# Performance work log

Measured on AMD Instinct MI355X. Metric: run time of the kernel, lower is better.

The kernel has to match this reference:

```python
import jax, jax.numpy as jnp
import numpy as np

B, S, IN_F, OUT_F = 4, 2048, 4096, 4096
ALPHA = 0.01

def setup_inputs() -> dict:
    key = jax.random.key(0)
    k1, k2 = jax.random.split(key, 2)
    # int8-valued activations and weights (stored as int32 per harness dtype)
    x = jax.random.randint(k1, (B, S, IN_F), -127, 127, dtype=jnp.int32)
    weight = jax.random.randint(k2, (IN_F, OUT_F), -127, 127, dtype=jnp.int32)
    bias = jnp.zeros((1, OUT_F), dtype=jnp.float16)
    alpha = jnp.full((1,), ALPHA, dtype=jnp.float32)
    return {"x": x, "weight": weight, "bias": bias, "alpha": alpha}

def reference(x, weight, bias, alpha):
    # Faithful to forward's default (non-hybrid) path:
    # y = F.linear(x.float(), weight.t().float(), bias.float()) * alpha
    # F.linear(x, W^T) == x @ W, with W shape (in_features, out_features).
    x_shape = x.shape
    xf = x.reshape(-1, x_shape[-1]).astype(jnp.float32)          # [B*S, in]
    wf = weight.astype(jnp.float32)                               # [in, out]
    y = (xf @ wf + bias.astype(jnp.float32)) * alpha              # [B*S, out]
    return y.reshape(*x_shape[:-1], -1)                           # [B, S, out]
```

## Files before the change

### kernel.cpp

```cpp
#include <hip/hip_runtime.h>
#include <hip/hip_fp16.h>

using i32x4  = __attribute__((ext_vector_type(4)))  int;
using i32x16 = __attribute__((ext_vector_type(16))) int;

static constexpr int M  = 4 * 2048;
static constexpr int N  = 4096;
static constexpr int K  = 4096;
static constexpr int BM = 128, BN = 128, BK = 64;
static constexpr int NT = K / BK;
static constexpr int TILE = BM * BK;


__device__ __forceinline__ unsigned pack4(i32x4 v) {
  return (unsigned)((v.x & 255) | ((v.y & 255) << 8) | ((v.z & 255) << 16) | (v.w << 24));
}

__global__ __launch_bounds__(256) void pack_x_kernel(const int* __restrict__ x,
                                                     unsigned char* __restrict__ wa) {
  unsigned g = blockIdx.x * 256 + threadIdx.x;
  unsigned tile = g >> 9, gt = g & 511;
  unsigned kg = gt >> 7, row = gt & 127;
  unsigned br = tile >> 6, kt = tile & 63;
  const int* src = x + ((size_t)(br * 128 + row) * K + kt * 64 + kg * 16);
  i32x4 v0 = *(const i32x4*)(src + 0);
  i32x4 v1 = *(const i32x4*)(src + 4);
  i32x4 v2 = *(const i32x4*)(src + 8);
  i32x4 v3 = *(const i32x4*)(src + 12);
  i32x4 d;
  d.x = (int)pack4(v0); d.y = (int)pack4(v1); d.z = (int)pack4(v2); d.w = (int)pack4(v3);
  *(i32x4*)(wa + (size_t)g * 16) = d;
}

__global__ __launch_bounds__(256) void pack_w_kernel(const int* __restrict__ w,
                                                     unsigned char* __restrict__ wb) {
  unsigned g = blockIdx.x * 256 + threadIdx.x;
  unsigned tile = g >> 9, gt = g & 511;
  unsigned kg = gt >> 7, col = gt & 127;
  unsigned bn = tile >> 6, kt = tile & 63;
  unsigned n  = bn * 128 + col;
  unsigned k0 = kt * 64 + kg * 16;
  const int* src = w + (size_t)k0 * N + n;
  i32x4 d;
#pragma unroll
  for (int j = 0; j < 4; ++j) {
    int b0 = src[(size_t)(j * 4 + 0) * N];
    int b1 = src[(size_t)(j * 4 + 1) * N];
    int b2 = src[(size_t)(j * 4 + 2) * N];
    int b3 = src[(size_t)(j * 4 + 3) * N];
    d[j] = (b0 & 255) | ((b1 & 255) << 8) | ((b2 & 255) << 16) | (b3 << 24);
  }
  *(i32x4*)(wb + (size_t)g * 16) = d;
}


__global__ __launch_bounds__(256) void gemm_i8(const unsigned char* __restrict__ wa,
                                               const unsigned char* __restrict__ wb,
                                               const __half* __restrict__ bias,
                                               const float* __restrict__ alphaP,
                                               float* __restrict__ out) {
  __shared__ __align__(16) unsigned char As[2][TILE];
  __shared__ __align__(16) unsigned char Bs[2][TILE];

  const int tid  = threadIdx.x;
  const int lane = tid & 63;
  const int w    = tid >> 6;
  const int wr   = w >> 1, wc = w & 1;
  const int l31  = lane & 31;
  const int kgl  = lane >> 5;

  const int bc = blockIdx.x;
  const int br = blockIdx.y;

  const unsigned char* ga = wa + (size_t)br * NT * TILE;
  const unsigned char* gb = wb + (size_t)bc * NT * TILE;

  i32x4 s0, s1, s2, s3;

#define GLOAD(T) do {                                                \
    const i32x4* ap = (const i32x4*)(ga + (size_t)(T) * TILE);       \
    const i32x4* bp = (const i32x4*)(gb + (size_t)(T) * TILE);       \
    s0 = ap[tid]; s1 = ap[tid + 256];                                \
    s2 = bp[tid]; s3 = bp[tid + 256];                                \
  } while (0)

#define SWRITE(BUF) do {                                             \
    i32x4* aw = (i32x4*)&As[BUF][0];                                 \
    i32x4* bw = (i32x4*)&Bs[BUF][0];                                 \
    aw[tid] = s0; aw[tid + 256] = s1;                                \
    bw[tid] = s2; bw[tid + 256] = s3;                                \
  } while (0)

  GLOAD(0);
  SWRITE(0);
  __syncthreads();

  i32x16 acc[2][2] = {};

  const int arow = wr * 64 + l31;
  const int bcol = wc * 64 + l31;

  for (int t = 0; t < NT; ++t) {
    const int cur = t & 1;
    if (t + 1 < NT) GLOAD(t + 1);

    const unsigned char* Ab = &As[cur][0] + kgl * 2048;
    const unsigned char* Bb = &Bs[cur][0] + kgl * 2048;
#pragma unroll
    for (int kc = 0; kc < 2; ++kc) {
      const unsigned char* Ap = Ab + kc * 4096;
      const unsigned char* Bp = Bb + kc * 4096;
      i32x4 a0 = *(const i32x4*)(Ap + (arow +  0) * 16);
      i32x4 a1 = *(const i32x4*)(Ap + (arow + 32) * 16);
      i32x4 b0 = *(const i32x4*)(Bp + (bcol +  0) * 16);
      i32x4 b1 = *(const i32x4*)(Bp + (bcol + 32) * 16);
      acc[0][0] = __builtin_amdgcn_mfma_i32_32x32x32_i8(a0, b0, acc[0][0], 0, 0, 0);
      acc[0][1] = __builtin_amdgcn_mfma_i32_32x32x32_i8(a0, b1, acc[0][1], 0, 0, 0);
      acc[1][0] = __builtin_amdgcn_mfma_i32_32x32x32_i8(a1, b0, acc[1][0], 0, 0, 0);
      acc[1][1] = __builtin_amdgcn_mfma_i32_32x32x32_i8(a1, b1, acc[1][1], 0, 0, 0);
    }

    __builtin_amdgcn_sched_barrier(0);
    if (t + 1 < NT) SWRITE(cur ^ 1);
    __syncthreads();
  }

  const float alpha = *alphaP;
  const int row0 = br * 128 + wr * 64 + 4 * kgl;
  const int col0 = bc * 128 + wc * 64 + l31;
#pragma unroll
  for (int ni = 0; ni < 2; ++ni) {
    const int col = col0 + ni * 32;
    const float bf = __half2float(bias[col]);
#pragma unroll
    for (int mi = 0; mi < 2; ++mi) {
#pragma unroll
      for (int r = 0; r < 16; ++r) {
        const int row = row0 + mi * 32 + (r & 3) + 8 * (r >> 2);
        out[(size_t)row * N + col] = ((float)acc[mi][ni][r] + bf) * alpha;
      }
    }
  }
#undef GLOAD
#undef SWRITE
}

extern "C" void kernel_launch(void* const* d_in, const int* in_sizes, int n_in,
                              void* d_out, int out_size, void* d_ws, size_t ws_size,
                              hipStream_t stream) {
  const int*    x     = (const int*)d_in[0];
  const int*    wgt   = (const int*)d_in[1];
  const __half* bias  = (const __half*)d_in[2];
  const float*  alpha = (const float*)d_in[3];
  float*        out   = (float*)d_out;

  unsigned char* wa = (unsigned char*)d_ws;
  unsigned char* wb = wa + (size_t)M * K;

  pack_x_kernel<<<(M * (size_t)K / 16) / 256, 256, 0, stream>>>(x, wa);
  pack_w_kernel<<<(N * (size_t)K / 16) / 256, 256, 0, stream>>>(wgt, wb);

  dim3 grid(N / BN, M / BM);
  gemm_i8<<<grid, 256, 0, stream>>>(wa, wb, bias, alpha, out);
}
```

Baseline: 230.4 us.

## Load B fragments directly to registers and merge pack kernels into one launch

The GEMM no longer stages the B tile through shared memory. Each wave loads its B MFMA fragments directly from the pre-packed global buffer into double-buffered registers, prefetched one k-tile ahead, with the main loop unrolled by two to select the register parity. This cuts LDS writes and reads and halves shared-memory usage, but duplicates B reads from global/L2 across waves and adds register pressure. The two packing kernels are also fused into one launch to remove a kernel boundary.

```diff
diff --git a/kernel.cpp b/kernel.cpp
--- a/kernel.cpp
+++ b/kernel.cpp
@@ -11,46 +11,49 @@
 static constexpr int NT = K / BK;
 static constexpr int TILE = BM * BK;
 
+static constexpr int PX_BLOCKS = (int)((size_t)M * K / 16 / 256);
+static constexpr int PW_BLOCKS = (int)((size_t)N * K / 16 / 256);
 
 __device__ __forceinline__ unsigned pack4(i32x4 v) {
   return (unsigned)((v.x & 255) | ((v.y & 255) << 8) | ((v.z & 255) << 16) | (v.w << 24));
 }
 
-__global__ __launch_bounds__(256) void pack_x_kernel(const int* __restrict__ x,
-                                                     unsigned char* __restrict__ wa) {
-  unsigned g = blockIdx.x * 256 + threadIdx.x;
-  unsigned tile = g >> 9, gt = g & 511;
-  unsigned kg = gt >> 7, row = gt & 127;
-  unsigned br = tile >> 6, kt = tile & 63;
-  const int* src = x + ((size_t)(br * 128 + row) * K + kt * 64 + kg * 16);
-  i32x4 v0 = *(const i32x4*)(src + 0);
-  i32x4 v1 = *(const i32x4*)(src + 4);
-  i32x4 v2 = *(const i32x4*)(src + 8);
-  i32x4 v3 = *(const i32x4*)(src + 12);
-  i32x4 d;
-  d.x = (int)pack4(v0); d.y = (int)pack4(v1); d.z = (int)pack4(v2); d.w = (int)pack4(v3);
-  *(i32x4*)(wa + (size_t)g * 16) = d;
-}
-
-__global__ __launch_bounds__(256) void pack_w_kernel(const int* __restrict__ w,
-                                                     unsigned char* __restrict__ wb) {
-  unsigned g = blockIdx.x * 256 + threadIdx.x;
-  unsigned tile = g >> 9, gt = g & 511;
-  unsigned kg = gt >> 7, col = gt & 127;
-  unsigned bn = tile >> 6, kt = tile & 63;
-  unsigned n  = bn * 128 + col;
-  unsigned k0 = kt * 64 + kg * 16;
-  const int* src = w + (size_t)k0 * N + n;
-  i32x4 d;
+__global__ __launch_bounds__(256) void pack_kernel(const int* __restrict__ x,
+                                                   const int* __restrict__ w,
+                                                   unsigned char* __restrict__ wa,
+                                                   unsigned char* __restrict__ wb) {
+  if (blockIdx.x < PX_BLOCKS) {
+    unsigned g = blockIdx.x * 256 + threadIdx.x;
+    unsigned tile = g >> 9, gt = g & 511;
+    unsigned kg = gt >> 7, row = gt & 127;
+    unsigned br = tile >> 6, kt = tile & 63;
+    const int* src = x + ((size_t)(br * 128 + row) * K + kt * 64 + kg * 16);
+    i32x4 v0 = *(const i32x4*)(src + 0);
+    i32x4 v1 = *(const i32x4*)(src + 4);
+    i32x4 v2 = *(const i32x4*)(src + 8);
+    i32x4 v3 = *(const i32x4*)(src + 12);
+    i32x4 d;
+    d.x = (int)pack4(v0); d.y = (int)pack4(v1); d.z = (int)pack4(v2); d.w = (int)pack4(v3);
+    *(i32x4*)(wa + (size_t)g * 16) = d;
+  } else {
+    unsigned g = (blockIdx.x - PX_BLOCKS) * 256 + threadIdx.x;
+    unsigned tile = g >> 9, gt = g & 511;
+    unsigned kg = gt >> 7, col = gt & 127;
+    unsigned bn = tile >> 6, kt = tile & 63;
+    unsigned n  = bn * 128 + col;
+    unsigned k0 = kt * 64 + kg * 16;
+    const int* src = w + (size_t)k0 * N + n;
+    i32x4 d;
 #pragma unroll
-  for (int j = 0; j < 4; ++j) {
-    int b0 = src[(size_t)(j * 4 + 0) * N];
-    int b1 = src[(size_t)(j * 4 + 1) * N];
-    int b2 = src[(size_t)(j * 4 + 2) * N];
-    int b3 = src[(size_t)(j * 4 + 3) * N];
-    d[j] = (b0 & 255) | ((b1 & 255) << 8) | ((b2 & 255) << 16) | (b3 << 24);
+    for (int j = 0; j < 4; ++j) {
+      int b0 = src[(size_t)(j * 4 + 0) * N];
+      int b1 = src[(size_t)(j * 4 + 1) * N];
+      int b2 = src[(size_t)(j * 4 + 2) * N];
+      int b3 = src[(size_t)(j * 4 + 3) * N];
+      d[j] = (b0 & 255) | ((b1 & 255) << 8) | ((b2 & 255) << 16) | (b3 << 24);
+    }
+    *(i32x4*)(wb + (size_t)g * 16) = d;
   }
-  *(i32x4*)(wb + (size_t)g * 16) = d;
 }
 
 
@@ -60,7 +63,6 @@
                                                const float* __restrict__ alphaP,
                                                float* __restrict__ out) {
   __shared__ __align__(16) unsigned char As[2][TILE];
-  __shared__ __align__(16) unsigned char Bs[2][TILE];
 
   const int tid  = threadIdx.x;
   const int lane = tid & 63;
@@ -75,54 +77,67 @@
   const unsigned char* ga = wa + (size_t)br * NT * TILE;
   const unsigned char* gb = wb + (size_t)bc * NT * TILE;
 
-  i32x4 s0, s1, s2, s3;
+  const int arow = wr * 64 + l31;
+  const int bcol = wc * 64 + l31;
 
-#define GLOAD(T) do {                                                \
+  i32x4 s0, s1;
+  i32x4 b[2][2][2];
+
+#define GLOADA(T) do {                                               \
     const i32x4* ap = (const i32x4*)(ga + (size_t)(T) * TILE);       \
-    const i32x4* bp = (const i32x4*)(gb + (size_t)(T) * TILE);       \
     s0 = ap[tid]; s1 = ap[tid + 256];                                \
-    s2 = bp[tid]; s3 = bp[tid + 256];                                \
+  } while (0)
+
+#define BLOAD(PAR, T) do {                                           \
+    const unsigned char* bt = gb + (size_t)(T) * TILE;               \
+    b[PAR][0][0] = *(const i32x4*)(bt + (kgl    ) * 2048 + (bcol +  0) * 16); \
+    b[PAR][0][1] = *(const i32x4*)(bt + (kgl    ) * 2048 + (bcol + 32) * 16); \
+    b[PAR][1][0] = *(const i32x4*)(bt + (kgl + 2) * 2048 + (bcol +  0) * 16); \
+    b[PAR][1][1] = *(const i32x4*)(bt + (kgl + 2) * 2048 + (bcol + 32) * 16); \
   } while (0)
 
 #define SWRITE(BUF) do {                                             \
     i32x4* aw = (i32x4*)&As[BUF][0];                                 \
-    i32x4* bw = (i32x4*)&Bs[BUF][0];                                 \
     aw[tid] = s0; aw[tid + 256] = s1;                                \
-    bw[tid] = s2; bw[tid + 256] = s3;                                \
   } while (0)
 
-  GLOAD(0);
+  GLOADA(0);
+  BLOAD(0, 0);
   SWRITE(0);
   __syncthreads();
 
   i32x16 acc[2][2] = {};
 
-  const int arow = wr * 64 + l31;
-  const int bcol = wc * 64 + l31;
+#define STEP(T, PAR) do {                                                      \
+    if ((T) + 1 < NT) { GLOADA((T) + 1); BLOAD(PAR ^ 1, (T) + 1); }            \
+    const unsigned char* Ab = &As[(T) & 1][0] + kgl * 2048;                    \
+    {                                                                          \
+      const unsigned char* Ap = Ab;                                   \
+      i32x4 a0 = *(const i32x4*)(Ap + (arow +  0) * 16);                       \
+      i32x4 a1 = *(const i32x4*)(Ap + (arow + 32) * 16);                       \
+      acc[0][0] = __builtin_amdgcn_mfma_i32_32x32x32_i8(a0, b[PAR][0][0], acc[0][0], 0, 0, 0); \
+      acc[0][1] = __builtin_amdgcn_mfma_i32_32x32x32_i8(a0, b[PAR][0][1], acc[0][1], 0, 0, 0); \
+      acc[1][0] = __builtin_amdgcn_mfma_i32_32x32x32_i8(a1, b[PAR][0][0], acc[1][0], 0, 0, 0); \
+      acc[1][1] = __builtin_amdgcn_mfma_i32_32x32x32_i8(a1, b[PAR][0][1], acc[1][1], 0, 0, 0); \
+    }                                                                          \
+    {                                                                          \
+      const unsigned char* Ap = Ab + 4096;                            \
+      i32x4 a0 = *(const i32x4*)(Ap + (arow +  0) * 16);                       \
+      i32x4 a1 = *(const i32x4*)(Ap + (arow + 32) * 16);                       \
+      acc[0][0] = __builtin_amdgcn_mfma_i32_32x32x32_i8(a0, b[PAR][1][0], acc[0][0], 0, 0, 0); \
+      acc[0][1] = __builtin_amdgcn_mfma_i32_32x32x32_i8(a0, b[PAR][1][1], acc[0][1], 0, 0, 0); \
+      acc[1][0] = __builtin_amdgcn_mfma_i32_32x32x32_i8(a1, b[PAR][1][0], acc[1][0], 0, 0, 0); \
+      acc[1][1] = __builtin_amdgcn_mfma_i32_32x32x32_i8(a1, b[PAR][1][1], acc[1][1], 0, 0, 0); \
+    }                                                                          \
+     \
+    __builtin_amdgcn_sched_barrier(0);                                         \
+    if ((T) + 1 < NT) SWRITE(((T) & 1) ^ 1);                                   \
+    __syncthreads();                                                           \
+  } while (0)
 
-  for (int t = 0; t < NT; ++t) {
-    const int cur = t & 1;
-    if (t + 1 < NT) GLOAD(t + 1);
-
-    const unsigned char* Ab = &As[cur][0] + kgl * 2048;
-    const unsigned char* Bb = &Bs[cur][0] + kgl * 2048;
-#pragma unroll
-    for (int kc = 0; kc < 2; ++kc) {
-      const unsigned char* Ap = Ab + kc * 4096;
-      const unsigned char* Bp = Bb + kc * 4096;
-      i32x4 a0 = *(const i32x4*)(Ap + (arow +  0) * 16);
-      i32x4 a1 = *(const i32x4*)(Ap + (arow + 32) * 16);
-      i32x4 b0 = *(const i32x4*)(Bp + (bcol +  0) * 16);
-      i32x4 b1 = *(const i32x4*)(Bp + (bcol + 32) * 16);
-      acc[0][0] = __builtin_amdgcn_mfma_i32_32x32x32_i8(a0, b0, acc[0][0], 0, 0, 0);
-      acc[0][1] = __builtin_amdgcn_mfma_i32_32x32x32_i8(a0, b1, acc[0][1], 0, 0, 0);
-      acc[1][0] = __builtin_amdgcn_mfma_i32_32x32x32_i8(a1, b0, acc[1][0], 0, 0, 0);
-      acc[1][1] = __builtin_amdgcn_mfma_i32_32x32x32_i8(a1, b1, acc[1][1], 0, 0, 0);
-    }
-
-    __builtin_amdgcn_sched_barrier(0);
-    if (t + 1 < NT) SWRITE(cur ^ 1);
-    __syncthreads();
+  for (int t = 0; t < NT; t += 2) {
+    STEP(t, 0);
+    STEP(t + 1, 1);
   }
 
   const float alpha = *alphaP;
@@ -141,7 +156,9 @@
       }
     }
   }
-#undef GLOAD
+#undef STEP
+#undef GLOADA
+#undef BLOAD
 #undef SWRITE
 }
 
@@ -157,8 +174,7 @@
   unsigned char* wa = (unsigned char*)d_ws;
   unsigned char* wb = wa + (size_t)M * K;
 
-  pack_x_kernel<<<(M * (size_t)K / 16) / 256, 256, 0, stream>>>(x, wa);
-  pack_w_kernel<<<(N * (size_t)K / 16) / 256, 256, 0, stream>>>(wgt, wb);
+  pack_kernel<<<PX_BLOCKS + PW_BLOCKS, 256, 0, stream>>>(x, wgt, wa, wb);
 
   dim3 grid(N / BN, M / BM);
   gemm_i8<<<grid, 256, 0, stream>>>(wa, wb, bias, alpha, out);
```

Measured after the change: 221.7 us. 3.8% less time.

## Drop LDS staging in int8 GEMM and merge pack kernels into one launch

Applied to the files above, without the earlier changes.

The GEMM no longer stages tiles through shared memory. Each wave loads its MFMA operands directly from the pre-packed global buffers into registers, software-prefetches the next K tile after issuing the MFMAs, and removes the __syncthreads barriers. The two pack kernels are merged into a single launch, and the GEMM gets a launch-bounds occupancy hint of 4 blocks. The trade is that operand reuse across waves now comes from L2/L1 instead of LDS, so global traffic per block rises in exchange for no barriers and higher occupancy.

```diff
diff --git a/kernel.cpp b/kernel.cpp
--- a/kernel.cpp
+++ b/kernel.cpp
@@ -7,61 +7,60 @@
 static constexpr int M  = 4 * 2048;
 static constexpr int N  = 4096;
 static constexpr int K  = 4096;
-static constexpr int BM = 128, BN = 128, BK = 64;
-static constexpr int NT = K / BK;
-static constexpr int TILE = BM * BK;
+static constexpr int NT = K / 64;
+static constexpr int TILE = 128 * 64;
 
+static constexpr int PX_BLOCKS = (int)((size_t)M * K / 16 / 256);
+static constexpr int PW_BLOCKS = (int)((size_t)N * K / 16 / 256);
 
 __device__ __forceinline__ unsigned pack4(i32x4 v) {
   return (unsigned)((v.x & 255) | ((v.y & 255) << 8) | ((v.z & 255) << 16) | (v.w << 24));
 }
 
-__global__ __launch_bounds__(256) void pack_x_kernel(const int* __restrict__ x,
-                                                     unsigned char* __restrict__ wa) {
-  unsigned g = blockIdx.x * 256 + threadIdx.x;
-  unsigned tile = g >> 9, gt = g & 511;
-  unsigned kg = gt >> 7, row = gt & 127;
-  unsigned br = tile >> 6, kt = tile & 63;
-  const int* src = x + ((size_t)(br * 128 + row) * K + kt * 64 + kg * 16);
-  i32x4 v0 = *(const i32x4*)(src + 0);
-  i32x4 v1 = *(const i32x4*)(src + 4);
-  i32x4 v2 = *(const i32x4*)(src + 8);
-  i32x4 v3 = *(const i32x4*)(src + 12);
-  i32x4 d;
-  d.x = (int)pack4(v0); d.y = (int)pack4(v1); d.z = (int)pack4(v2); d.w = (int)pack4(v3);
-  *(i32x4*)(wa + (size_t)g * 16) = d;
-}
-
-__global__ __launch_bounds__(256) void pack_w_kernel(const int* __restrict__ w,
-                                                     unsigned char* __restrict__ wb) {
-  unsigned g = blockIdx.x * 256 + threadIdx.x;
-  unsigned tile = g >> 9, gt = g & 511;
-  unsigned kg = gt >> 7, col = gt & 127;
-  unsigned bn = tile >> 6, kt = tile & 63;
-  unsigned n  = bn * 128 + col;
-  unsigned k0 = kt * 64 + kg * 16;
-  const int* src = w + (size_t)k0 * N + n;
-  i32x4 d;
+__global__ __launch_bounds__(256) void pack_kernel(const int* __restrict__ x,
+                                                   const int* __restrict__ w,
+                                                   unsigned char* __restrict__ wa,
+                                                   unsigned char* __restrict__ wb) {
+  if (blockIdx.x < PX_BLOCKS) {
+    unsigned g = blockIdx.x * 256 + threadIdx.x;
+    unsigned tile = g >> 9, gt = g & 511;
+    unsigned kg = gt >> 7, row = gt & 127;
+    unsigned br = tile >> 6, kt = tile & 63;
+    const int* src = x + ((size_t)(br * 128 + row) * K + kt * 64 + kg * 16);
+    i32x4 v0 = *(const i32x4*)(src + 0);
+    i32x4 v1 = *(const i32x4*)(src + 4);
+    i32x4 v2 = *(const i32x4*)(src + 8);
+    i32x4 v3 = *(const i32x4*)(src + 12);
+    i32x4 d;
+    d.x = (int)pack4(v0); d.y = (int)pack4(v1); d.z = (int)pack4(v2); d.w = (int)pack4(v3);
+    *(i32x4*)(wa + (size_t)g * 16) = d;
+  } else {
+    unsigned g = (blockIdx.x - PX_BLOCKS) * 256 + threadIdx.x;
+    unsigned tile = g >> 9, gt = g & 511;
+    unsigned kg = gt >> 7, col = gt & 127;
+    unsigned bn = tile >> 6, kt = tile & 63;
+    unsigned n  = bn * 128 + col;
+    unsigned k0 = kt * 64 + kg * 16;
+    const int* src = w + (size_t)k0 * N + n;
+    i32x4 d;
 #pragma unroll
-  for (int j = 0; j < 4; ++j) {
-    int b0 = src[(size_t)(j * 4 + 0) * N];
-    int b1 = src[(size_t)(j * 4 + 1) * N];
-    int b2 = src[(size_t)(j * 4 + 2) * N];
-    int b3 = src[(size_t)(j * 4 + 3) * N];
-    d[j] = (b0 & 255) | ((b1 & 255) << 8) | ((b2 & 255) << 16) | (b3 << 24);
+    for (int j = 0; j < 4; ++j) {
+      int b0 = src[(size_t)(j * 4 + 0) * N];
+      int b1 = src[(size_t)(j * 4 + 1) * N];
+      int b2 = src[(size_t)(j * 4 + 2) * N];
+      int b3 = src[(size_t)(j * 4 + 3) * N];
+      d[j] = (b0 & 255) | ((b1 & 255) << 8) | ((b2 & 255) << 16) | (b3 << 24);
+    }
+    *(i32x4*)(wb + (size_t)g * 16) = d;
   }
-  *(i32x4*)(wb + (size_t)g * 16) = d;
 }
 
 
-__global__ __launch_bounds__(256) void gemm_i8(const unsigned char* __restrict__ wa,
-                                               const unsigned char* __restrict__ wb,
-                                               const __half* __restrict__ bias,
-                                               const float* __restrict__ alphaP,
-                                               float* __restrict__ out) {
-  __shared__ __align__(16) unsigned char As[2][TILE];
-  __shared__ __align__(16) unsigned char Bs[2][TILE];
-
+__global__ __launch_bounds__(256, 4) void gemm_i8(const unsigned char* __restrict__ wa,
+                                                  const unsigned char* __restrict__ wb,
+                                                  const __half* __restrict__ bias,
+                                                  const float* __restrict__ alphaP,
+                                                  float* __restrict__ out) {
   const int tid  = threadIdx.x;
   const int lane = tid & 63;
   const int w    = tid >> 6;
@@ -72,57 +71,39 @@
   const int bc = blockIdx.x;
   const int br = blockIdx.y;
 
-  const unsigned char* ga = wa + (size_t)br * NT * TILE;
-  const unsigned char* gb = wb + (size_t)bc * NT * TILE;
+  const unsigned char* gaw = wa + (size_t)br * NT * TILE;
+  const unsigned char* gbw = wb + (size_t)bc * NT * TILE;
 
-  i32x4 s0, s1, s2, s3;
+  const int aoff = kgl * 2048 + (wr * 64 + l31) * 16;
+  const int boff = kgl * 2048 + (wc * 64 + l31) * 16;
 
-#define GLOAD(T) do {                                                \
-    const i32x4* ap = (const i32x4*)(ga + (size_t)(T) * TILE);       \
-    const i32x4* bp = (const i32x4*)(gb + (size_t)(T) * TILE);       \
-    s0 = ap[tid]; s1 = ap[tid + 256];                                \
-    s2 = bp[tid]; s3 = bp[tid + 256];                                \
+  i32x4 a0, a1, b0, b1, c0, c1, d0, d1;
+
+#define LOADT(T) do {                                                \
+    const unsigned char* at = gaw + (size_t)(T) * TILE;              \
+    const unsigned char* bt = gbw + (size_t)(T) * TILE;              \
+    a0 = *(const i32x4*)(at + aoff);                                 \
+    a1 = *(const i32x4*)(at + aoff + 512);                           \
+    b0 = *(const i32x4*)(bt + boff);                                 \
+    b1 = *(const i32x4*)(bt + boff + 512);                           \
+    c0 = *(const i32x4*)(at + 4096 + aoff);                          \
+    c1 = *(const i32x4*)(at + 4096 + aoff + 512);                    \
+    d0 = *(const i32x4*)(bt + 4096 + boff);                          \
+    d1 = *(const i32x4*)(bt + 4096 + boff + 512);                    \
   } while (0)
-
-#define SWRITE(BUF) do {                                             \
-    i32x4* aw = (i32x4*)&As[BUF][0];                                 \
-    i32x4* bw = (i32x4*)&Bs[BUF][0];                                 \
-    aw[tid] = s0; aw[tid + 256] = s1;                                \
-    bw[tid] = s2; bw[tid + 256] = s3;                                \
-  } while (0)
-
-  GLOAD(0);
-  SWRITE(0);
-  __syncthreads();
 
   i32x16 acc[2][2] = {};
 
-  const int arow = wr * 64 + l31;
-  const int bcol = wc * 64 + l31;
+#define MF(mi, ni, A, B) \
+  acc[mi][ni] = __builtin_amdgcn_mfma_i32_32x32x32_i8(A, B, acc[mi][ni], 0, 0, 0)
 
+  LOADT(0);
   for (int t = 0; t < NT; ++t) {
-    const int cur = t & 1;
-    if (t + 1 < NT) GLOAD(t + 1);
-
-    const unsigned char* Ab = &As[cur][0] + kgl * 2048;
-    const unsigned char* Bb = &Bs[cur][0] + kgl * 2048;
-#pragma unroll
-    for (int kc = 0; kc < 2; ++kc) {
-      const unsigned char* Ap = Ab + kc * 4096;
-      const unsigned char* Bp = Bb + kc * 4096;
-      i32x4 a0 = *(const i32x4*)(Ap + (arow +  0) * 16);
-      i32x4 a1 = *(const i32x4*)(Ap + (arow + 32) * 16);
-      i32x4 b0 = *(const i32x4*)(Bp + (bcol +  0) * 16);
-      i32x4 b1 = *(const i32x4*)(Bp + (bcol + 32) * 16);
-      acc[0][0] = __builtin_amdgcn_mfma_i32_32x32x32_i8(a0, b0, acc[0][0], 0, 0, 0);
-      acc[0][1] = __builtin_amdgcn_mfma_i32_32x32x32_i8(a0, b1, acc[0][1], 0, 0, 0);
-      acc[1][0] = __builtin_amdgcn_mfma_i32_32x32x32_i8(a1, b0, acc[1][0], 0, 0, 0);
-      acc[1][1] = __builtin_amdgcn_mfma_i32_32x32x32_i8(a1, b1, acc[1][1], 0, 0, 0);
-    }
-
-    __builtin_amdgcn_sched_barrier(0);
-    if (t + 1 < NT) SWRITE(cur ^ 1);
-    __syncthreads();
+    MF(0, 0, a0, b0); MF(0, 1, a0, b1);
+    MF(1, 0, a1, b0); MF(1, 1, a1, b1);
+    MF(0, 0, c0, d0); MF(0, 1, c0, d1);
+    MF(1, 0, c1, d0); MF(1, 1, c1, d1);
+    if (t + 1 < NT) LOADT(t + 1);
   }
 
   const float alpha = *alphaP;
@@ -141,8 +122,8 @@
       }
     }
   }
-#undef GLOAD
-#undef SWRITE
+#undef MF
+#undef LOADT
 }
 
 extern "C" void kernel_launch(void* const* d_in, const int* in_sizes, int n_in,
@@ -157,9 +138,8 @@
   unsigned char* wa = (unsigned char*)d_ws;
   unsigned char* wb = wa + (size_t)M * K;
 
-  pack_x_kernel<<<(M * (size_t)K / 16) / 256, 256, 0, stream>>>(x, wa);
-  pack_w_kernel<<<(N * (size_t)K / 16) / 256, 256, 0, stream>>>(wgt, wb);
+  pack_kernel<<<PX_BLOCKS + PW_BLOCKS, 256, 0, stream>>>(x, wgt, wa, wb);
 
-  dim3 grid(N / BN, M / BM);
+  dim3 grid(N / 128, M / 128);
   gemm_i8<<<grid, 256, 0, stream>>>(wa, wb, bias, alpha, out);
 }
```

New measurement: 235.4 us. +2.1%, slower.
